# Optimization experiments

Measured on AMD Instinct MI355X. Metric: run time of the kernel, lower is better.

Reference implementation:

```python
import jax, jax.numpy as jnp
import numpy as np

N_NODES = 100000
N_EDGES = 600000
IN_DIM = 128
HID = 128
OUT_DIM = 64
N_LAYERS = 3


def setup_inputs() -> dict:
    key = jax.random.key(0)
    ks = jax.random.split(key, 8)
    x = jax.random.normal(ks[0], (N_NODES, IN_DIM), dtype=jnp.float32)
    edge_index = jax.random.randint(ks[1], (2, N_EDGES), 0, N_NODES, dtype=jnp.int64)
    s = 1.0 / np.sqrt(HID)
    W_in = jax.random.normal(ks[2], (HID, IN_DIM), dtype=jnp.float32) * s
    b_in = jax.random.normal(ks[3], (HID,), dtype=jnp.float32) * s
    W_convs = jax.random.normal(ks[4], (N_LAYERS, HID, HID), dtype=jnp.float32) * s
    b_convs = jax.random.normal(ks[5], (N_LAYERS, HID), dtype=jnp.float32) * s
    W_out = jax.random.normal(ks[6], (OUT_DIM, (N_LAYERS + 1) * HID), dtype=jnp.float32) * s
    b_out = jax.random.normal(ks[7], (OUT_DIM,), dtype=jnp.float32) * s
    return {"x": x, "edge_index": edge_index, "W_in": W_in, "b_in": b_in,
            "W_convs": W_convs, "b_convs": b_convs, "W_out": W_out, "b_out": b_out}


def reference(x, edge_index, W_in, b_in, W_convs, b_convs, W_out, b_out):
    src, dst = edge_index[0], edge_index[1]
    n = x.shape[0]
    # input projection: [N, in] -> [N, H]
    h = x @ W_in.T + b_in
    hidden_states = [h]
    for i in range(W_convs.shape[0]):
        # GINConv (eps=0): nn(x + sum of neighbor messages), messages src->dst
        agg = jax.ops.segment_sum(h[src], dst, num_segments=n)
        h = (h + agg) @ W_convs[i].T + b_convs[i]
        hidden_states.append(h)
    cat = jnp.concatenate(hidden_states, axis=1)  # [N, (L+1)*H]
    out = cat @ W_out.T + b_out  # [N, OUT]
    return jax.nn.softmax(out, axis=-1)
```

## Files before the change

### kernel.cpp

```cpp
#include <hip/hip_runtime.h>
#include <hip/hip_bf16.h>
#include <hip/hip_fp16.h>

#define GN 100000
#define GE 600000
#define SCAN_NBLK 98

typedef __bf16    bf16x8 __attribute__((ext_vector_type(8)));
typedef __bf16    bf16x4 __attribute__((ext_vector_type(4)));
typedef _Float16  f16x8  __attribute__((ext_vector_type(8)));
typedef float     f32x4  __attribute__((ext_vector_type(4)));

__global__ __launch_bounds__(256) void convert_w(
    const float* __restrict__ Win, const float* __restrict__ Wc,
    const float* __restrict__ Wout,
    __bf16* __restrict__ hi, __bf16* __restrict__ lo)
{
    const int i = blockIdx.x * 256 + threadIdx.x;
    if (i >= 98304) return;
    float v;
    if (i < 16384)      v = Win[i];
    else if (i < 65536) v = Wc[i - 16384];
    else                v = Wout[i - 65536];
    const __bf16 h = (__bf16)v;
    hi[i] = h;
    lo[i] = (__bf16)(v - (float)h);
}

template<bool GATHER>
__global__ __launch_bounds__(512, 4) void gin_layer(
    const float* __restrict__ H, int ldH,
    const _Float16* __restrict__ HfIn,
    const int* __restrict__ row_start,
    const int* __restrict__ deg,
    const int* __restrict__ csr,
    const __bf16* __restrict__ Whi,
    const __bf16* __restrict__ Wlo,
    const float* __restrict__ bias,
    float* __restrict__ C, int ldC,
    _Float16* __restrict__ HfOut)
{
    constexpr int K   = 128;
    constexpr int ALD = 132;

    __shared__ float Acc[64 * ALD];

    const int tid  = threadIdx.x;
    const int wave = tid >> 6;
    const int lane = tid & 63;
    const int row0 = blockIdx.x * 64;
    const int wm   = (wave >> 2) * 32;
    const int wn   = (wave & 3) * 32;
    const int quad = lane >> 4;
    const int l15  = lane & 15;

#pragma unroll
    for (int p = 0; p < 4; ++p) {
        const int q  = tid + p * 512;
        const int r  = q >> 5;
        const int c4 = (q & 31) * 4;
        float4 v = make_float4(0.f, 0.f, 0.f, 0.f);
        if (row0 + r < GN) v = *(const float4*)(H + (size_t)(row0 + r) * ldH + c4);
        *(float4*)&Acc[r * ALD + c4] = v;
    }

    if (GATHER) {
        const uint* Hw = (const uint*)HfIn;
        float2 acc8[8];
        int start8[8], deg8[8];
        int maxd = 0;
#pragma unroll
        for (int r = 0; r < 8; ++r) {
            acc8[r] = make_float2(0.f, 0.f);
            const int v = row0 + wave * 8 + r;
            start8[r] = (v < GN) ? row_start[v] : 0;
            deg8[r]   = (v < GN) ? deg[v] : 0;
            maxd = max(maxd, deg8[r]);
        }
        int scur[8];
#pragma unroll
        for (int r = 0; r < 8; ++r) {
            const int s = csr[start8[r]];
            scur[r] = min(max(s, 0), GN - 1);
        }
        for (int k = 0; k < maxd; ++k) {
            int snext[8];
#pragma unroll
            for (int r = 0; r < 8; ++r) {
                const int kk = max(min(k + 1, deg8[r] - 1), 0);
                snext[r] = csr[start8[r] + kk];
            }
            uint t[8];
#pragma unroll
            for (int r = 0; r < 8; ++r)
                t[r] = Hw[(size_t)scur[r] * 64 + lane];
#pragma unroll
            for (int r = 0; r < 8; ++r) {
                const float m = (k < deg8[r]) ? 1.f : 0.f;
                union { uint u; _Float16 h[2]; } cv;
                cv.u = t[r];
                acc8[r].x = fmaf(m, (float)cv.h[0], acc8[r].x);
                acc8[r].y = fmaf(m, (float)cv.h[1], acc8[r].y);
                scur[r] = min(max(snext[r], 0), GN - 1);
            }
        }
        __syncthreads();
        const int j = lane * 2;
#pragma unroll
        for (int r = 0; r < 8; ++r) {
            float* a = &Acc[(wave * 8 + r) * ALD + j];
            a[0] += acc8[r].x;
            a[1] += acc8[r].y;
        }
    }
    __syncthreads();

    f32x4 acc[2][2];
#pragma unroll
    for (int i = 0; i < 2; ++i)
#pragma unroll
        for (int j = 0; j < 2; ++j) acc[i][j] = (f32x4)(0.0f);

#pragma unroll
    for (int ks = 0; ks < 4; ++ks) {
        const int kt = ks * 32 + quad * 8;
        bf16x8 ahi[2], alo[2];
#pragma unroll
        for (int mt = 0; mt < 2; ++mt) {
            const float* ap = &Acc[(wm + mt * 16 + l15) * ALD + kt];
            const f32x4 p = *(const f32x4*)ap;
            const f32x4 q = *(const f32x4*)(ap + 4);
#pragma unroll
            for (int e = 0; e < 4; ++e) {
                const __bf16 hp = (__bf16)p[e];
                const __bf16 hq = (__bf16)q[e];
                ahi[mt][e]     = hp;
                ahi[mt][e + 4] = hq;
                alo[mt][e]     = (__bf16)(p[e] - (float)hp);
                alo[mt][e + 4] = (__bf16)(q[e] - (float)hq);
            }
        }
        bf16x8 whi[2], wlo[2];
#pragma unroll
        for (int nt = 0; nt < 2; ++nt) {
            const int n = wn + nt * 16 + l15;
            whi[nt] = *(const bf16x8*)(Whi + (size_t)n * K + kt);
            wlo[nt] = *(const bf16x8*)(Wlo + (size_t)n * K + kt);
        }
#pragma unroll
        for (int mt = 0; mt < 2; ++mt)
#pragma unroll
            for (int nt = 0; nt < 2; ++nt) {
                acc[mt][nt] = __builtin_amdgcn_mfma_f32_16x16x32_bf16(
                    ahi[mt], whi[nt], acc[mt][nt], 0, 0, 0);
                acc[mt][nt] = __builtin_amdgcn_mfma_f32_16x16x32_bf16(
                    ahi[mt], wlo[nt], acc[mt][nt], 0, 0, 0);
                acc[mt][nt] = __builtin_amdgcn_mfma_f32_16x16x32_bf16(
                    alo[mt], whi[nt], acc[mt][nt], 0, 0, 0);
            }
    }
    __syncthreads();

#pragma unroll
    for (int nt = 0; nt < 2; ++nt) {
        const int col = wn + nt * 16 + l15;
        const float b = bias[col];
#pragma unroll
        for (int mt = 0; mt < 2; ++mt)
#pragma unroll
            for (int r4 = 0; r4 < 4; ++r4)
                Acc[(wm + mt * 16 + quad * 4 + r4) * ALD + col] = acc[mt][nt][r4] + b;
    }
    __syncthreads();
#pragma unroll
    for (int p = 0; p < 4; ++p) {
        const int q  = tid + p * 512;
        const int r  = q >> 5;
        const int c4 = (q & 31) * 4;
        const int gr = row0 + r;
        if (gr < GN)
            *(float4*)(C + (size_t)gr * ldC + c4) = *(const float4*)&Acc[r * ALD + c4];
    }
#pragma unroll
    for (int p = 0; p < 2; ++p) {
        const int q = tid + p * 512;
        const int r = q >> 4;
        const int g = (q & 15) * 8;
        const int gr = row0 + r;
        if (gr < GN) {
            const float4 a = *(const float4*)&Acc[r * ALD + g];
            const float4 b = *(const float4*)&Acc[r * ALD + g + 4];
            f16x8 o = {(_Float16)a.x, (_Float16)a.y, (_Float16)a.z, (_Float16)a.w,
                       (_Float16)b.x, (_Float16)b.y, (_Float16)b.z, (_Float16)b.w};
            *(f16x8*)&HfOut[(size_t)gr * 128 + g] = o;
        }
    }
}

__global__ __launch_bounds__(512, 4) void gin_final(
    const float* __restrict__ cat3,
    const _Float16* __restrict__ HfIn,
    const int* __restrict__ row_start,
    const int* __restrict__ deg,
    const int* __restrict__ csr,
    const __bf16* __restrict__ Whi3,
    const __bf16* __restrict__ Wlo3,
    const float* __restrict__ b3,
    const __bf16* __restrict__ WhiO,
    const __bf16* __restrict__ WloO,
    const float* __restrict__ bO,
    float* __restrict__ out)
{
    constexpr int ALD = 132;
    constexpr int CLD = 68;

    __shared__ float Acc[64 * ALD];
    __shared__ float Cst[64 * CLD];

    const int tid  = threadIdx.x;
    const int wave = tid >> 6;
    const int lane = tid & 63;
    const int row0 = blockIdx.x * 64;
    const int quad = lane >> 4;
    const int l15  = lane & 15;

#pragma unroll
    for (int p = 0; p < 4; ++p) {
        const int q  = tid + p * 512;
        const int r  = q >> 5;
        const int c4 = (q & 31) * 4;
        float4 v = make_float4(0.f, 0.f, 0.f, 0.f);
        if (row0 + r < GN)
            v = *(const float4*)(cat3 + (size_t)(row0 + r) * 384 + 256 + c4);
        *(float4*)&Acc[r * ALD + c4] = v;
    }

    {
        const uint* Hw = (const uint*)HfIn;
        float2 acc8[8];
        int start8[8], deg8[8];
        int maxd = 0;
#pragma unroll
        for (int r = 0; r < 8; ++r) {
            acc8[r] = make_float2(0.f, 0.f);
            const int v = row0 + wave * 8 + r;
            start8[r] = (v < GN) ? row_start[v] : 0;
            deg8[r]   = (v < GN) ? deg[v] : 0;
            maxd = max(maxd, deg8[r]);
        }
        int scur[8];
#pragma unroll
        for (int r = 0; r < 8; ++r) {
            const int s = csr[start8[r]];
            scur[r] = min(max(s, 0), GN - 1);
        }
        for (int k = 0; k < maxd; ++k) {
            int snext[8];
#pragma unroll
            for (int r = 0; r < 8; ++r) {
                const int kk = max(min(k + 1, deg8[r] - 1), 0);
                snext[r] = csr[start8[r] + kk];
            }
            uint t[8];
#pragma unroll
            for (int r = 0; r < 8; ++r)
                t[r] = Hw[(size_t)scur[r] * 64 + lane];
#pragma unroll
            for (int r = 0; r < 8; ++r) {
                const float m = (k < deg8[r]) ? 1.f : 0.f;
                union { uint u; _Float16 h[2]; } cv;
                cv.u = t[r];
                acc8[r].x = fmaf(m, (float)cv.h[0], acc8[r].x);
                acc8[r].y = fmaf(m, (float)cv.h[1], acc8[r].y);
                scur[r] = min(max(snext[r], 0), GN - 1);
            }
        }
        __syncthreads();
        const int j = lane * 2;
#pragma unroll
        for (int r = 0; r < 8; ++r) {
            float* a = &Acc[(wave * 8 + r) * ALD + j];
            a[0] += acc8[r].x;
            a[1] += acc8[r].y;
        }
    }
    __syncthreads();

    const int wm = (wave >> 2) * 32;
    const int wn = (wave & 3) * 32;
    f32x4 acc1[2][2];
#pragma unroll
    for (int i = 0; i < 2; ++i)
#pragma unroll
        for (int j = 0; j < 2; ++j) acc1[i][j] = (f32x4)(0.0f);

#pragma unroll
    for (int ks = 0; ks < 4; ++ks) {
        const int kt = ks * 32 + quad * 8;
        bf16x8 ahi[2], alo[2];
#pragma unroll
        for (int mt = 0; mt < 2; ++mt) {
            const float* ap = &Acc[(wm + mt * 16 + l15) * ALD + kt];
            const f32x4 p = *(const f32x4*)ap;
            const f32x4 q = *(const f32x4*)(ap + 4);
#pragma unroll
            for (int e = 0; e < 4; ++e) {
                const __bf16 hp = (__bf16)p[e];
                const __bf16 hq = (__bf16)q[e];
                ahi[mt][e]     = hp;
                ahi[mt][e + 4] = hq;
                alo[mt][e]     = (__bf16)(p[e] - (float)hp);
                alo[mt][e + 4] = (__bf16)(q[e] - (float)hq);
            }
        }
        bf16x8 whi[2], wlo[2];
#pragma unroll
        for (int nt = 0; nt < 2; ++nt) {
            const int n = wn + nt * 16 + l15;
            whi[nt] = *(const bf16x8*)(Whi3 + (size_t)n * 128 + kt);
            wlo[nt] = *(const bf16x8*)(Wlo3 + (size_t)n * 128 + kt);
        }
#pragma unroll
        for (int mt = 0; mt < 2; ++mt)
#pragma unroll
            for (int nt = 0; nt < 2; ++nt) {
                acc1[mt][nt] = __builtin_amdgcn_mfma_f32_16x16x32_bf16(
                    ahi[mt], whi[nt], acc1[mt][nt], 0, 0, 0);
                acc1[mt][nt] = __builtin_amdgcn_mfma_f32_16x16x32_bf16(
                    ahi[mt], wlo[nt], acc1[mt][nt], 0, 0, 0);
                acc1[mt][nt] = __builtin_amdgcn_mfma_f32_16x16x32_bf16(
                    alo[mt], whi[nt], acc1[mt][nt], 0, 0, 0);
            }
    }
    __syncthreads();

#pragma unroll
    for (int nt = 0; nt < 2; ++nt) {
        const int col = wn + nt * 16 + l15;
        const float b = b3[col];
#pragma unroll
        for (int mt = 0; mt < 2; ++mt)
#pragma unroll
            for (int r4 = 0; r4 < 4; ++r4)
                Acc[(wm + mt * 16 + quad * 4 + r4) * ALD + col] = acc1[mt][nt][r4] + b;
    }
    __syncthreads();

    const int wk  = wave & 1;
    const int wn2 = ((wave >> 1) & 1) * 32;
    const int wm2 = ((wave >> 2) & 1) * 32;
    f32x4 acc2[2][2];
#pragma unroll
    for (int i = 0; i < 2; ++i)
#pragma unroll
        for (int j = 0; j < 2; ++j) acc2[i][j] = (f32x4)(0.0f);

#pragma unroll
    for (int ks = 0; ks < 8; ++ks) {
        const int kg = wk * 256 + ks * 32 + quad * 8;
        bf16x8 ahi[2], alo[2];
#pragma unroll
        for (int mt = 0; mt < 2; ++mt) {
            const int row = wm2 + mt * 16 + l15;
            f32x4 p, q;
            if (kg < 384) {
                const float* ap = cat3 + (size_t)(row0 + row) * 384 + kg;
                p = *(const f32x4*)ap;
                q = *(const f32x4*)(ap + 4);
            } else {
                const float* ap = &Acc[row * ALD + (kg - 384)];
                p = *(const f32x4*)ap;
                q = *(const f32x4*)(ap + 4);
            }
#pragma unroll
            for (int e = 0; e < 4; ++e) {
                const __bf16 hp = (__bf16)p[e];
                const __bf16 hq = (__bf16)q[e];
                ahi[mt][e]     = hp;
                ahi[mt][e + 4] = hq;
                alo[mt][e]     = (__bf16)(p[e] - (float)hp);
                alo[mt][e + 4] = (__bf16)(q[e] - (float)hq);
            }
        }
        bf16x8 whi[2], wlo[2];
#pragma unroll
        for (int nt = 0; nt < 2; ++nt) {
            const int n = wn2 + nt * 16 + l15;
            whi[nt] = *(const bf16x8*)(WhiO + (size_t)n * 512 + kg);
            wlo[nt] = *(const bf16x8*)(WloO + (size_t)n * 512 + kg);
        }
#pragma unroll
        for (int mt = 0; mt < 2; ++mt)
#pragma unroll
            for (int nt = 0; nt < 2; ++nt) {
                acc2[mt][nt] = __builtin_amdgcn_mfma_f32_16x16x32_bf16(
                    ahi[mt], whi[nt], acc2[mt][nt], 0, 0, 0);
                acc2[mt][nt] = __builtin_amdgcn_mfma_f32_16x16x32_bf16(
                    ahi[mt], wlo[nt], acc2[mt][nt], 0, 0, 0);
                acc2[mt][nt] = __builtin_amdgcn_mfma_f32_16x16x32_bf16(
                    alo[mt], whi[nt], acc2[mt][nt], 0, 0, 0);
            }
    }

    if (wk == 1) {
#pragma unroll
        for (int nt = 0; nt < 2; ++nt)
#pragma unroll
            for (int mt = 0; mt < 2; ++mt)
#pragma unroll
                for (int r4 = 0; r4 < 4; ++r4)
                    Cst[(wm2 + mt * 16 + quad * 4 + r4) * CLD + wn2 + nt * 16 + l15]
                        = acc2[mt][nt][r4];
    }
    __syncthreads();
    if (wk == 0) {
#pragma unroll
        for (int nt = 0; nt < 2; ++nt) {
            const int col = wn2 + nt * 16 + l15;
            const float b = bO[col];
#pragma unroll
            for (int mt = 0; mt < 2; ++mt)
#pragma unroll
                for (int r4 = 0; r4 < 4; ++r4) {
                    const int idx = (wm2 + mt * 16 + quad * 4 + r4) * CLD + col;
                    Cst[idx] = Cst[idx] + acc2[mt][nt][r4] + b;
                }
        }
    }
    __syncthreads();

    for (int i = 0; i < 8; ++i) {
        const int r = wave * 8 + i;
        const float v = Cst[r * CLD + lane];
        float m = v;
#pragma unroll
        for (int off = 32; off > 0; off >>= 1) m = fmaxf(m, __shfl_xor(m, off));
        const float e = __expf(v - m);
        float s = e;
#pragma unroll
        for (int off = 32; off > 0; off >>= 1) s += __shfl_xor(s, off);
        const int gr = row0 + r;
        if (gr < GN) out[(size_t)gr * 64 + lane] = e / s;
    }
}

__global__ __launch_bounds__(256) void count_deg(const int* __restrict__ dst,
                                                 int* __restrict__ deg)
{
    const int e = blockIdx.x * 256 + threadIdx.x;
    if (e < GE) atomicAdd(&deg[dst[e]], 1);
}

__global__ __launch_bounds__(256) void scan_pass1(const int* __restrict__ deg,
                                                  int* __restrict__ excl,
                                                  int* __restrict__ blockSums)
{
    __shared__ int s[256];
    const int t = threadIdx.x;
    const int base = blockIdx.x * 1024 + t * 4;

    int4 v = make_int4(0, 0, 0, 0);
    if (base + 3 < GN) {
        v = *(const int4*)(deg + base);
    } else {
        if (base + 0 < GN) v.x = deg[base + 0];
        if (base + 1 < GN) v.y = deg[base + 1];
        if (base + 2 < GN) v.z = deg[base + 2];
        if (base + 3 < GN) v.w = deg[base + 3];
    }
    const int mysum = v.x + v.y + v.z + v.w;
    s[t] = mysum;
    __syncthreads();
    for (int off = 1; off < 256; off <<= 1) {
        const int val = (t >= off) ? s[t - off] : 0;
        __syncthreads();
        s[t] += val;
        __syncthreads();
    }
    int4 o;
    o.x = s[t] - mysum;
    o.y = o.x + v.x;
    o.z = o.y + v.y;
    o.w = o.z + v.z;
    if (base + 3 < GN) {
        *(int4*)(excl + base) = o;
    } else {
        if (base + 0 < GN) excl[base + 0] = o.x;
        if (base + 1 < GN) excl[base + 1] = o.y;
        if (base + 2 < GN) excl[base + 2] = o.z;
        if (base + 3 < GN) excl[base + 3] = o.w;
    }
    if (t == 255) blockSums[blockIdx.x] = s[255];
}

__global__ __launch_bounds__(128) void scan_pass2(const int* __restrict__ blockSums,
                                                  int* __restrict__ blockOffs, int n)
{
    __shared__ int s[128];
    const int t = threadIdx.x;
    const int v = (t < n) ? blockSums[t] : 0;
    s[t] = v;
    __syncthreads();
    for (int off = 1; off < 128; off <<= 1) {
        const int val = (t >= off) ? s[t - off] : 0;
        __syncthreads();
        s[t] += val;
        __syncthreads();
    }
    if (t < n) blockOffs[t] = s[t] - v;
}

__global__ __launch_bounds__(256) void scan_pass3(int* __restrict__ excl,
                                                  const int* __restrict__ blockOffs,
                                                  int* __restrict__ cursor)
{
    const int i = blockIdx.x * 256 + threadIdx.x;
    if (i >= GN) return;
    const int v = excl[i] + blockOffs[i >> 10];
    excl[i]   = v;
    cursor[i] = v;
}

__global__ __launch_bounds__(256) void fill_csr(const int* __restrict__ src,
                                                const int* __restrict__ dst,
                                                int* __restrict__ cursor,
                                                int* __restrict__ csr)
{
    const int e = blockIdx.x * 256 + threadIdx.x;
    if (e >= GE) return;
    const int pos = atomicAdd(&cursor[dst[e]], 1);
    csr[pos] = src[e];
}

extern "C" void kernel_launch(void* const* d_in, const int* in_sizes, int n_in,
                              void* d_out, int out_size, void* d_ws, size_t ws_size,
                              hipStream_t stream)
{
    const float* x       = (const float*)d_in[0];
    const int*   src     = (const int*)d_in[1];
    const int*   dst     = ((const int*)d_in[1]) + GE;
    const float* W_in    = (const float*)d_in[2];
    const float* b_in    = (const float*)d_in[3];
    const float* W_convs = (const float*)d_in[4];
    const float* b_convs = (const float*)d_in[5];
    const float* W_out   = (const float*)d_in[6];
    const float* b_out   = (const float*)d_in[7];
    float*       out     = (float*)d_out;

    float*    cat3 = (float*)d_ws;
    _Float16* Hf0  = (_Float16*)(cat3 + (size_t)GN * 384);
    _Float16* Hf1  = Hf0 + (size_t)GN * 128;
    int*      deg       = (int*)(Hf1 + (size_t)GN * 128);
    int*      row_start = deg + GN;
    int*      cursor    = row_start + GN;
    int*      blockSums = cursor + GN;
    int*      blockOffs = blockSums + 128;
    int*      csr       = blockOffs + 128;
    __bf16*   Whi       = (__bf16*)(csr + GE);
    __bf16*   Wlo       = Whi + 98304;

    const dim3 blk(256);
    const dim3 gblk(512);
    const int edge_blocks  = (GE + 255) / 256;
    const int node_blocks  = (GN + 255) / 256;
    const int layer_blocks = (GN + 63) / 64;

    hipMemsetAsync(deg, 0, GN * sizeof(int), stream);
    count_deg<<<edge_blocks, blk, 0, stream>>>(dst, deg);
    scan_pass1<<<SCAN_NBLK, blk, 0, stream>>>(deg, row_start, blockSums);
    scan_pass2<<<1, 128, 0, stream>>>(blockSums, blockOffs, SCAN_NBLK);
    scan_pass3<<<node_blocks, blk, 0, stream>>>(row_start, blockOffs, cursor);
    fill_csr<<<edge_blocks, blk, 0, stream>>>(src, dst, cursor, csr);

    convert_w<<<(98304 + 255) / 256, blk, 0, stream>>>(W_in, W_convs, W_out, Whi, Wlo);

    gin_layer<false><<<layer_blocks, gblk, 0, stream>>>(
        x, 128, nullptr, nullptr, nullptr, nullptr,
        Whi, Wlo, b_in, cat3, 384, Hf0);

    gin_layer<true><<<layer_blocks, gblk, 0, stream>>>(
        cat3, 384, Hf0, row_start, deg, csr,
        Whi + 16384, Wlo + 16384, b_convs, cat3 + 128, 384, Hf1);
    gin_layer<true><<<layer_blocks, gblk, 0, stream>>>(
        cat3 + 128, 384, Hf1, row_start, deg, csr,
        Whi + 32768, Wlo + 32768, b_convs + 128, cat3 + 256, 384, Hf0);

    gin_final<<<layer_blocks, gblk, 0, stream>>>(
        cat3, Hf0, row_start, deg, csr,
        Whi + 49152, Wlo + 49152, b_convs + 256,
        Whi + 65536, Wlo + 65536, b_out, out);
}
```

Before: 526.0 us.

## Software-pipeline neighbor gather two edges deep and raise occupancy

Factors the CSR neighbor gather into a shared helper that prefetches two edges ahead, unrolled by two, and drops the per-step index clamping. It relies on a zeroed pad after the CSR array so over-reads past a row land on node 0, and masks those contributions with a select instead of an FMA. Launch bounds go from 4 to 8 waves-per-EU hints, and gin_final aliases its two LDS buffers with an extra barrier to cut shared memory. The goal is more memory-level parallelism on the latency-bound gather. The cost is more register pressure and dependence on the padding; an over-read at a row boundary reads the next row's CSR entries, which is harmless because the mask discards them.

```diff
diff --git a/kernel.cpp b/kernel.cpp
--- a/kernel.cpp
+++ b/kernel.cpp
@@ -5,6 +5,8 @@
 #define GN 100000
 #define GE 600000
 #define SCAN_NBLK 98
+#define ALD 132
+#define CSR_PAD 256
 
 typedef __bf16    bf16x8 __attribute__((ext_vector_type(8)));
 typedef __bf16    bf16x4 __attribute__((ext_vector_type(4)));
@@ -27,8 +29,81 @@
     lo[i] = (__bf16)(v - (float)h);
 }
 
+__device__ __forceinline__ void gather8_f16(
+    const uint* __restrict__ Hw,
+    const int* __restrict__ row_start,
+    const int* __restrict__ deg,
+    const int* __restrict__ csr,
+    const int row0, const int wave, const int lane,
+    float* __restrict__ Acc)
+{
+    float2 acc8[8];
+    int pc8[8], dg8[8];
+    int maxd = 0;
+#pragma unroll
+    for (int r = 0; r < 8; ++r) {
+        acc8[r] = make_float2(0.f, 0.f);
+        const int v = row0 + wave * 8 + r;
+        pc8[r] = (v < GN) ? row_start[v] : 0;
+        dg8[r] = (v < GN) ? deg[v] : 0;
+        maxd = max(maxd, dg8[r]);
+    }
+
+    int sA[8], sB[8];
+#pragma unroll
+    for (int r = 0; r < 8; ++r) sA[r] = csr[pc8[r]];
+#pragma unroll
+    for (int r = 0; r < 8; ++r) sB[r] = csr[pc8[r] + 1];
+#pragma unroll
+    for (int r = 0; r < 8; ++r) pc8[r] += 2;
+    uint tA[8];
+#pragma unroll
+    for (int r = 0; r < 8; ++r) tA[r] = Hw[(size_t)sA[r] * 64 + lane];
+
+    for (int k = 0; k < maxd; k += 2) {
+        int sN[8];
+#pragma unroll
+        for (int r = 0; r < 8; ++r) sN[r] = csr[pc8[r]];
+        uint tB[8];
+#pragma unroll
+        for (int r = 0; r < 8; ++r) tB[r] = Hw[(size_t)sB[r] * 64 + lane];
+#pragma unroll
+        for (int r = 0; r < 8; ++r) {
+            union { uint u; _Float16 h[2]; } cv;
+            cv.u = (k < dg8[r]) ? tA[r] : 0u;
+            acc8[r].x += (float)cv.h[0];
+            acc8[r].y += (float)cv.h[1];
+        }
+        int sM[8];
+#pragma unroll
+        for (int r = 0; r < 8; ++r) sM[r] = csr[pc8[r] + 1];
+#pragma unroll
+        for (int r = 0; r < 8; ++r) pc8[r] += 2;
+#pragma unroll
+        for (int r = 0; r < 8; ++r) tA[r] = Hw[(size_t)sN[r] * 64 + lane];
+#pragma unroll
+        for (int r = 0; r < 8; ++r) {
+            union { uint u; _Float16 h[2]; } cv;
+            cv.u = (k + 1 < dg8[r]) ? tB[r] : 0u;
+            acc8[r].x += (float)cv.h[0];
+            acc8[r].y += (float)cv.h[1];
+        }
+#pragma unroll
+        for (int r = 0; r < 8; ++r) sB[r] = sM[r];
+    }
+
+    __syncthreads();
+    const int j = lane * 2;
+#pragma unroll
+    for (int r = 0; r < 8; ++r) {
+        float* a = &Acc[(wave * 8 + r) * ALD + j];
+        a[0] += acc8[r].x;
+        a[1] += acc8[r].y;
+    }
+}
+
 template<bool GATHER>
-__global__ __launch_bounds__(512, 4) void gin_layer(
+__global__ __launch_bounds__(512, 8) void gin_layer(
     const float* __restrict__ H, int ldH,
     const _Float16* __restrict__ HfIn,
     const int* __restrict__ row_start,
@@ -40,8 +115,7 @@
     float* __restrict__ C, int ldC,
     _Float16* __restrict__ HfOut)
 {
-    constexpr int K   = 128;
-    constexpr int ALD = 132;
+    constexpr int K = 128;
 
     __shared__ float Acc[64 * ALD];
 
@@ -64,55 +138,8 @@
         *(float4*)&Acc[r * ALD + c4] = v;
     }
 
-    if (GATHER) {
-        const uint* Hw = (const uint*)HfIn;
-        float2 acc8[8];
-        int start8[8], deg8[8];
-        int maxd = 0;
-#pragma unroll
-        for (int r = 0; r < 8; ++r) {
-            acc8[r] = make_float2(0.f, 0.f);
-            const int v = row0 + wave * 8 + r;
-            start8[r] = (v < GN) ? row_start[v] : 0;
-            deg8[r]   = (v < GN) ? deg[v] : 0;
-            maxd = max(maxd, deg8[r]);
-        }
-        int scur[8];
-#pragma unroll
-        for (int r = 0; r < 8; ++r) {
-            const int s = csr[start8[r]];
-            scur[r] = min(max(s, 0), GN - 1);
-        }
-        for (int k = 0; k < maxd; ++k) {
-            int snext[8];
-#pragma unroll
-            for (int r = 0; r < 8; ++r) {
-                const int kk = max(min(k + 1, deg8[r] - 1), 0);
-                snext[r] = csr[start8[r] + kk];
-            }
-            uint t[8];
-#pragma unroll
-            for (int r = 0; r < 8; ++r)
-                t[r] = Hw[(size_t)scur[r] * 64 + lane];
-#pragma unroll
-            for (int r = 0; r < 8; ++r) {
-                const float m = (k < deg8[r]) ? 1.f : 0.f;
-                union { uint u; _Float16 h[2]; } cv;
-                cv.u = t[r];
-                acc8[r].x = fmaf(m, (float)cv.h[0], acc8[r].x);
-                acc8[r].y = fmaf(m, (float)cv.h[1], acc8[r].y);
-                scur[r] = min(max(snext[r], 0), GN - 1);
-            }
-        }
-        __syncthreads();
-        const int j = lane * 2;
-#pragma unroll
-        for (int r = 0; r < 8; ++r) {
-            float* a = &Acc[(wave * 8 + r) * ALD + j];
-            a[0] += acc8[r].x;
-            a[1] += acc8[r].y;
-        }
-    }
+    if (GATHER)
+        gather8_f16((const uint*)HfIn, row_start, deg, csr, row0, wave, lane, Acc);
     __syncthreads();
 
     f32x4 acc[2][2];
@@ -197,7 +224,7 @@
     }
 }
 
-__global__ __launch_bounds__(512, 4) void gin_final(
+__global__ __launch_bounds__(512, 8) void gin_final(
     const float* __restrict__ cat3,
     const _Float16* __restrict__ HfIn,
     const int* __restrict__ row_start,
@@ -211,11 +238,11 @@
     const float* __restrict__ bO,
     float* __restrict__ out)
 {
-    constexpr int ALD = 132;
     constexpr int CLD = 68;
 
-    __shared__ float Acc[64 * ALD];
-    __shared__ float Cst[64 * CLD];
+    __shared__ float Smem[64 * ALD];
+    float* const Acc = Smem;
+    float* const Cst = Smem;
 
     const int tid  = threadIdx.x;
     const int wave = tid >> 6;
@@ -235,55 +262,7 @@
         *(float4*)&Acc[r * ALD + c4] = v;
     }
 
-    {
-        const uint* Hw = (const uint*)HfIn;
-        float2 acc8[8];
-        int start8[8], deg8[8];
-        int maxd = 0;
-#pragma unroll
-        for (int r = 0; r < 8; ++r) {
-            acc8[r] = make_float2(0.f, 0.f);
-            const int v = row0 + wave * 8 + r;
-            start8[r] = (v < GN) ? row_start[v] : 0;
-            deg8[r]   = (v < GN) ? deg[v] : 0;
-            maxd = max(maxd, deg8[r]);
-        }
-        int scur[8];
-#pragma unroll
-        for (int r = 0; r < 8; ++r) {
-            const int s = csr[start8[r]];
-            scur[r] = min(max(s, 0), GN - 1);
-        }
-        for (int k = 0; k < maxd; ++k) {
-            int snext[8];
-#pragma unroll
-            for (int r = 0; r < 8; ++r) {
-                const int kk = max(min(k + 1, deg8[r] - 1), 0);
-                snext[r] = csr[start8[r] + kk];
-            }
-            uint t[8];
-#pragma unroll
-            for (int r = 0; r < 8; ++r)
-                t[r] = Hw[(size_t)scur[r] * 64 + lane];
-#pragma unroll
-            for (int r = 0; r < 8; ++r) {
-                const float m = (k < deg8[r]) ? 1.f : 0.f;
-                union { uint u; _Float16 h[2]; } cv;
-                cv.u = t[r];
-                acc8[r].x = fmaf(m, (float)cv.h[0], acc8[r].x);
-                acc8[r].y = fmaf(m, (float)cv.h[1], acc8[r].y);
-                scur[r] = min(max(snext[r], 0), GN - 1);
-            }
-        }
-        __syncthreads();
-        const int j = lane * 2;
-#pragma unroll
-        for (int r = 0; r < 8; ++r) {
-            float* a = &Acc[(wave * 8 + r) * ALD + j];
-            a[0] += acc8[r].x;
-            a[1] += acc8[r].y;
-        }
-    }
+    gather8_f16((const uint*)HfIn, row_start, deg, csr, row0, wave, lane, Acc);
     __syncthreads();
 
     const int wm = (wave >> 2) * 32;
@@ -401,6 +380,8 @@
                     alo[mt], whi[nt], acc2[mt][nt], 0, 0, 0);
             }
     }
+
+    __syncthreads();
 
     if (wk == 1) {
 #pragma unroll
@@ -556,7 +537,7 @@
     int*      blockSums = cursor + GN;
     int*      blockOffs = blockSums + 128;
     int*      csr       = blockOffs + 128;
-    __bf16*   Whi       = (__bf16*)(csr + GE);
+    __bf16*   Whi       = (__bf16*)(csr + GE + CSR_PAD);
     __bf16*   Wlo       = Whi + 98304;
 
     const dim3 blk(256);
@@ -566,6 +547,7 @@
     const int layer_blocks = (GN + 63) / 64;
 
     hipMemsetAsync(deg, 0, GN * sizeof(int), stream);
+    hipMemsetAsync(csr + GE, 0, CSR_PAD * sizeof(int), stream);
     count_deg<<<edge_blocks, blk, 0, stream>>>(dst, deg);
     scan_pass1<<<SCAN_NBLK, blk, 0, stream>>>(deg, row_start, blockSums);
     scan_pass2<<<1, 128, 0, stream>>>(blockSums, blockOffs, SCAN_NBLK);
```

Result: slower. 964.6 us (+83.4%).
